# Optimization experiments

Measured on AMD Instinct MI355X. Metric: run time of the kernel, lower is better.

## Reference

```python
import jax, jax.numpy as jnp
import numpy as np

EPS = 1e-5  # BatchNorm2d default eps


def setup_inputs() -> dict:
    key = jax.random.key(0)
    ks = jax.random.split(key, 6)
    B, C, H, W = 32, 6, 512, 512
    IC = 3  # inter_channels = channels // r
    x = jax.random.normal(ks[0], (B, C, H, W), dtype=jnp.float32)
    # conv1: 1x1 conv C->IC  (stored as [out, in])
    w1 = jax.random.normal(ks[1], (IC, C), dtype=jnp.float32) * (1.0 / np.sqrt(C))
    b1 = jnp.zeros((IC,), dtype=jnp.float32)
    # BN1 (inference-style params)
    g1 = jnp.ones((IC,), jnp.float32)
    be1 = jnp.zeros((IC,), jnp.float32)
    m1 = jax.random.normal(ks[2], (IC,), dtype=jnp.float32) * 0.1
    v1 = jax.random.uniform(ks[3], (IC,), dtype=jnp.float32, minval=0.5, maxval=1.5)
    # conv2: 1x1 conv IC->C
    w2 = jax.random.normal(ks[4], (C, IC), dtype=jnp.float32) * (1.0 / np.sqrt(IC))
    b2 = jnp.zeros((C,), dtype=jnp.float32)
    # BN2
    g2 = jnp.ones((C,), jnp.float32)
    be2 = jnp.zeros((C,), jnp.float32)
    m2 = jax.random.normal(ks[5], (C,), dtype=jnp.float32) * 0.1
    v2 = jnp.ones((C,), jnp.float32)
    return {"x": x, "w1": w1, "b1": b1, "g1": g1, "be1": be1, "m1": m1, "v1": v1,
            "w2": w2, "b2": b2, "g2": g2, "be2": be2, "m2": m2, "v2": v2}


def _bn(h, g, be, m, v):
    # inference BatchNorm over channel axis 1
    inv = g * jax.lax.rsqrt(v + EPS)
    return h * inv[None, :, None, None] + (be - m * inv)[None, :, None, None]


def reference(x, w1, b1, g1, be1, m1, v1, w2, b2, g2, be2, m2, v2):
    # local_att: 1x1 conv -> BN -> ReLU -> 1x1 conv -> BN
    h = jnp.einsum('bchw,oc->bohw', x, w1) + b1[None, :, None, None]
    h = jax.nn.relu(_bn(h, g1, be1, m1, v1))
    h = jnp.einsum('bchw,oc->bohw', h, w2) + b2[None, :, None, None]
    h = _bn(h, g2, be2, m2, v2)
    # softmax over channel dim (view(b, num_features, -1) + softmax dim=1 == channel softmax)
    w = jax.nn.softmax(h, axis=1)
    # chunk + per-channel multiply + stack + sum == sum over channels of x*w
    out = jnp.sum(x * w, axis=1)  # [B, H, W]  (squeeze(1) of [B,1,H,W])
    return out
```

## Files before the change

### kernel.cpp

```cpp
#include <hip/hip_runtime.h>

#define HW_SHIFT 18
#define HW (1 << HW_SHIFT)
#define NC 6
#define NIC 3
#define EPS 1e-5f

__global__ __launch_bounds__(256) void aff_softmax_kernel(
    const float* __restrict__ x,
    const float* __restrict__ w1, const float* __restrict__ b1,
    const float* __restrict__ g1, const float* __restrict__ be1,
    const float* __restrict__ m1, const float* __restrict__ v1,
    const float* __restrict__ w2, const float* __restrict__ b2,
    const float* __restrict__ g2, const float* __restrict__ be2,
    const float* __restrict__ m2, const float* __restrict__ v2,
    float* __restrict__ out)
{
    const int g = blockIdx.x * blockDim.x + threadIdx.x;

    float W1f[NIC][NC], B1f[NIC];
#pragma unroll
    for (int o = 0; o < NIC; ++o) {
        const float inv = g1[o] * rsqrtf(v1[o] + EPS);
        B1f[o] = b1[o] * inv + (be1[o] - m1[o] * inv);
#pragma unroll
        for (int c = 0; c < NC; ++c) W1f[o][c] = w1[o * NC + c] * inv;
    }
    float W2f[NC][NIC], B2f[NC];
#pragma unroll
    for (int o = 0; o < NC; ++o) {
        const float inv = g2[o] * rsqrtf(v2[o] + EPS);
        B2f[o] = b2[o] * inv + (be2[o] - m2[o] * inv);
#pragma unroll
        for (int c = 0; c < NIC; ++c) W2f[o][c] = w2[o * NIC + c] * inv;
    }

    const long p  = (long)g << 2;
    const int  b  = (int)(p >> HW_SHIFT);
    const int  hw = (int)(p & (HW - 1));
    const float* xb = x + ((long)b * NC << HW_SHIFT) + hw;

    float4 xv[NC];
#pragma unroll
    for (int c = 0; c < NC; ++c)
        xv[c] = *(const float4*)(xb + ((long)c << HW_SHIFT));

    float4 res;
    float* resf = (float*)&res;
#pragma unroll
    for (int i = 0; i < 4; ++i) {
        float xc[NC];
#pragma unroll
        for (int c = 0; c < NC; ++c) xc[c] = ((const float*)&xv[c])[i];

        float h1[NIC];
#pragma unroll
        for (int o = 0; o < NIC; ++o) {
            float a = B1f[o];
#pragma unroll
            for (int c = 0; c < NC; ++c) a = fmaf(W1f[o][c], xc[c], a);
            h1[o] = fmaxf(a, 0.0f);
        }

        float h2[NC];
        float mx = -3.4e38f;
#pragma unroll
        for (int o = 0; o < NC; ++o) {
            float a = B2f[o];
#pragma unroll
            for (int c = 0; c < NIC; ++c) a = fmaf(W2f[o][c], h1[c], a);
            h2[o] = a;
            mx = fmaxf(mx, a);
        }

        float sum = 0.0f, acc = 0.0f;
#pragma unroll
        for (int o = 0; o < NC; ++o) {
            const float e = __expf(h2[o] - mx);
            sum += e;
            acc = fmaf(e, xc[o], acc);
        }
        resf[i] = acc / sum;
    }

    *(float4*)(out + p) = res;
}

extern "C" void kernel_launch(void* const* d_in, const int* in_sizes, int n_in,
                              void* d_out, int out_size, void* d_ws, size_t ws_size,
                              hipStream_t stream) {
    const float* x   = (const float*)d_in[0];
    const float* w1  = (const float*)d_in[1];
    const float* b1  = (const float*)d_in[2];
    const float* g1  = (const float*)d_in[3];
    const float* be1 = (const float*)d_in[4];
    const float* m1  = (const float*)d_in[5];
    const float* v1  = (const float*)d_in[6];
    const float* w2  = (const float*)d_in[7];
    const float* b2  = (const float*)d_in[8];
    const float* g2  = (const float*)d_in[9];
    const float* be2 = (const float*)d_in[10];
    const float* m2  = (const float*)d_in[11];
    const float* v2  = (const float*)d_in[12];
    float* out = (float*)d_out;

    const int threads = 256;
    const int total4  = out_size / 4;
    const int blocks  = (total4 + threads - 1) / threads;

    aff_softmax_kernel<<<blocks, threads, 0, stream>>>(
        x, w1, b1, g1, be1, m1, v1, w2, b2, g2, be2, m2, v2, out);
}
```

Measured before the change: 302.4 us.

## Use grid-stride loop with nontemporal loads/stores and uniform folded weights

Caps the grid at 2048 blocks and turns the kernel into a grid-stride loop, so the folded conv/BN weights are computed once per thread instead of once per four outputs. Input loads and output stores use nontemporal builtins to avoid polluting the cache on this streaming workload. Folded weights are forced into scalar registers via readfirstlane, and the division is replaced with a hardware reciprocal. In exchange, fewer resident waves may hide less memory latency, and the approximate reciprocal slightly loosens precision.

Result: no change. 299.2 us (-1.1%).

```diff
diff --git a/kernel.cpp b/kernel.cpp
--- a/kernel.cpp
+++ b/kernel.cpp
@@ -6,7 +6,13 @@
 #define NIC 3
 #define EPS 1e-5f
 
-__global__ __launch_bounds__(256) void aff_softmax_kernel(
+typedef float f4 __attribute__((ext_vector_type(4)));
+
+__device__ __forceinline__ float uniform_f(float v) {
+    return __uint_as_float(__builtin_amdgcn_readfirstlane(__float_as_uint(v)));
+}
+
+__global__ __launch_bounds__(256, 8) void aff_softmax_kernel(
     const float* __restrict__ x,
     const float* __restrict__ w1, const float* __restrict__ b1,
     const float* __restrict__ g1, const float* __restrict__ be1,
@@ -14,76 +20,71 @@
     const float* __restrict__ w2, const float* __restrict__ b2,
     const float* __restrict__ g2, const float* __restrict__ be2,
     const float* __restrict__ m2, const float* __restrict__ v2,
-    float* __restrict__ out)
+    float* __restrict__ out, int total4)
 {
-    const int g = blockIdx.x * blockDim.x + threadIdx.x;
-
     float W1f[NIC][NC], B1f[NIC];
 #pragma unroll
     for (int o = 0; o < NIC; ++o) {
         const float inv = g1[o] * rsqrtf(v1[o] + EPS);
-        B1f[o] = b1[o] * inv + (be1[o] - m1[o] * inv);
+        B1f[o] = uniform_f(fmaf(b1[o], inv, be1[o] - m1[o] * inv));
 #pragma unroll
-        for (int c = 0; c < NC; ++c) W1f[o][c] = w1[o * NC + c] * inv;
+        for (int c = 0; c < NC; ++c) W1f[o][c] = uniform_f(w1[o * NC + c] * inv);
     }
     float W2f[NC][NIC], B2f[NC];
 #pragma unroll
     for (int o = 0; o < NC; ++o) {
         const float inv = g2[o] * rsqrtf(v2[o] + EPS);
-        B2f[o] = b2[o] * inv + (be2[o] - m2[o] * inv);
+        B2f[o] = uniform_f(fmaf(b2[o], inv, be2[o] - m2[o] * inv));
 #pragma unroll
-        for (int c = 0; c < NIC; ++c) W2f[o][c] = w2[o * NIC + c] * inv;
+        for (int c = 0; c < NIC; ++c) W2f[o][c] = uniform_f(w2[o * NIC + c] * inv);
     }
 
-    const long p  = (long)g << 2;
-    const int  b  = (int)(p >> HW_SHIFT);
-    const int  hw = (int)(p & (HW - 1));
-    const float* xb = x + ((long)b * NC << HW_SHIFT) + hw;
+    const int stride = gridDim.x * blockDim.x;
+    for (int g = blockIdx.x * blockDim.x + threadIdx.x; g < total4; g += stride) {
+        const int p  = g << 2;
+        const int b  = p >> HW_SHIFT;
+        const int hw = p & (HW - 1);
+        const float* xb = x + ((long)(b * NC) << HW_SHIFT) + hw;
 
-    float4 xv[NC];
+        f4 xv[NC];
 #pragma unroll
-    for (int c = 0; c < NC; ++c)
-        xv[c] = *(const float4*)(xb + ((long)c << HW_SHIFT));
+        for (int c = 0; c < NC; ++c)
+            xv[c] = __builtin_nontemporal_load((const f4*)(xb + (c << HW_SHIFT)));
 
-    float4 res;
-    float* resf = (float*)&res;
+        f4 res;
 #pragma unroll
-    for (int i = 0; i < 4; ++i) {
-        float xc[NC];
+        for (int i = 0; i < 4; ++i) {
+            float h1[NIC];
 #pragma unroll
-        for (int c = 0; c < NC; ++c) xc[c] = ((const float*)&xv[c])[i];
+            for (int o = 0; o < NIC; ++o) {
+                float a = B1f[o];
+#pragma unroll
+                for (int c = 0; c < NC; ++c) a = fmaf(W1f[o][c], xv[c][i], a);
+                h1[o] = fmaxf(a, 0.0f);
+            }
 
-        float h1[NIC];
+            float h2[NC], mx = -3.4e38f;
 #pragma unroll
-        for (int o = 0; o < NIC; ++o) {
-            float a = B1f[o];
+            for (int o = 0; o < NC; ++o) {
+                float a = B2f[o];
 #pragma unroll
-            for (int c = 0; c < NC; ++c) a = fmaf(W1f[o][c], xc[c], a);
-            h1[o] = fmaxf(a, 0.0f);
+                for (int c = 0; c < NIC; ++c) a = fmaf(W2f[o][c], h1[c], a);
+                h2[o] = a;
+                mx = fmaxf(mx, a);
+            }
+
+            float sum = 0.0f, acc = 0.0f;
+#pragma unroll
+            for (int o = 0; o < NC; ++o) {
+                const float e = __expf(h2[o] - mx);
+                sum += e;
+                acc = fmaf(e, xv[o][i], acc);
+            }
+            res[i] = acc * __builtin_amdgcn_rcpf(sum);
         }
 
-        float h2[NC];
-        float mx = -3.4e38f;
-#pragma unroll
-        for (int o = 0; o < NC; ++o) {
-            float a = B2f[o];
-#pragma unroll
-            for (int c = 0; c < NIC; ++c) a = fmaf(W2f[o][c], h1[c], a);
-            h2[o] = a;
-            mx = fmaxf(mx, a);
-        }
-
-        float sum = 0.0f, acc = 0.0f;
-#pragma unroll
-        for (int o = 0; o < NC; ++o) {
-            const float e = __expf(h2[o] - mx);
-            sum += e;
-            acc = fmaf(e, xc[o], acc);
-        }
-        resf[i] = acc / sum;
+        __builtin_nontemporal_store(res, (f4*)(out + p));
     }
-
-    *(float4*)(out + p) = res;
 }
 
 extern "C" void kernel_launch(void* const* d_in, const int* in_sizes, int n_in,
@@ -106,8 +107,10 @@
 
     const int threads = 256;
     const int total4  = out_size / 4;
-    const int blocks  = (total4 + threads - 1) / threads;
+    int blocks = 2048;
+    const int needed = (total4 + threads - 1) / threads;
+    if (blocks > needed) blocks = needed;
 
     aff_softmax_kernel<<<blocks, threads, 0, stream>>>(
-        x, w1, b1, g1, be1, m1, v1, w2, b2, g2, be2, m2, v2, out);
+        x, w1, b1, g1, be1, m1, v1, w2, b2, g2, be2, m2, v2, out, total4);
 }
```
